# Kernel optimization log

Measured on AMD Instinct MI355X. Metric: run time of the kernel, lower is better.

The kernel has to match this reference:

```python
import jax, jax.numpy as jnp
import numpy as np

DIM = 64
HEADS = 4
EPS_LN = 1e-6
EPS_NORM = 1e-12


def _dwconv(x, w):
    # depthwise 3x3, SAME padding; x: [B,C,H,W], w: [C,1,3,3]
    return jax.lax.conv_general_dilated(
        x, w, window_strides=(1, 1), padding='SAME',
        feature_group_count=x.shape[1],
        dimension_numbers=('NCHW', 'OIHW', 'NCHW'))


def setup_inputs() -> dict:
    key = jax.random.key(0)
    ks = jax.random.split(key, 10)
    s = 0.05
    inp = {
        'x': jax.random.normal(ks[0], (8, DIM, 256, 256), dtype=jnp.float32),
        'ln_w': jnp.ones((DIM,), jnp.float32),
        'ln_b': jnp.zeros((DIM,), jnp.float32),
        'w_q': jax.random.normal(ks[1], (DIM, DIM), jnp.float32) * s,
        'w_k': jax.random.normal(ks[2], (DIM, DIM), jnp.float32) * s,
        'w_v': jax.random.normal(ks[3], (DIM, DIM), jnp.float32) * s,
        'dw_q': jax.random.normal(ks[4], (DIM, 1, 3, 3), jnp.float32) * s,
        'dw_k': jax.random.normal(ks[5], (DIM, 1, 3, 3), jnp.float32) * s,
        'dw_v': jax.random.normal(ks[6], (DIM, 1, 3, 3), jnp.float32) * s,
        'w_proj': jax.random.normal(ks[7], (DIM, DIM, 3, 3), jnp.float32) * s,
        'w_comp': jax.random.normal(ks[8], (DIM // 4, DIM), jnp.float32) * s,
        'temperature': jnp.ones((HEADS, 1, 1), jnp.float32),
    }
    return inp


def reference(x, ln_w, ln_b, w_q, w_k, w_v, dw_q, dw_k, dw_v, w_proj, w_comp, temperature):
    b, c, h, w = x.shape
    heads = temperature.shape[0]
    hd = c // heads  # per-head channels

    # LayerNorm over channel dim (per spatial location), biased variance
    mu = jnp.mean(x, axis=1, keepdims=True)
    var = jnp.mean((x - mu) ** 2, axis=1, keepdims=True)
    xn = (x - mu) / jnp.sqrt(var + EPS_LN)
    xn = xn * ln_w[None, :, None, None] + ln_b[None, :, None, None]

    # 1x1 projections then depthwise 3x3
    q = _dwconv(jnp.einsum('oc,bchw->bohw', w_q, xn), dw_q)
    k = _dwconv(jnp.einsum('oc,bchw->bohw', w_k, xn), dw_k)
    v = _dwconv(jnp.einsum('oc,bchw->bohw', w_v, xn), dw_v)

    # [b, heads, hd, h*w]
    q = q.reshape(b, heads, hd, h * w)
    k = k.reshape(b, heads, hd, h * w)
    v = v.reshape(b, heads, hd, h * w)

    # L2 normalize along spatial axis (torch F.normalize: x / max(||x||, eps))
    q = q / jnp.maximum(jnp.linalg.norm(q, axis=-1, keepdims=True), EPS_NORM)
    k = k / jnp.maximum(jnp.linalg.norm(k, axis=-1, keepdims=True), EPS_NORM)

    # channel attention: [b, heads, hd, hd]
    attn = jnp.einsum('bhcn,bhdn->bhcd', q, k) * temperature[None]
    attn = jax.nn.softmax(attn, axis=-1)
    out = jnp.einsum('bhcd,bhdn->bhcn', attn, v).reshape(b, c, h, w)

    # 3x3 projection + residual (residual is the normalized x, per source)
    out = jax.lax.conv_general_dilated(
        out, w_proj, window_strides=(1, 1), padding='SAME',
        dimension_numbers=('NCHW', 'OIHW', 'NCHW')) + xn

    # 1x1 compress to dim//4
    return jnp.einsum('oc,bchw->bohw', w_comp, out)
```

## Files before the change

kernel.cpp:

```cpp
#include <hip/hip_runtime.h>
#include <hip/hip_bf16.h>
#include <stdint.h>

#define BB 8
#define CC 64
#define HH 256
#define WW 256
#define NPIX 65536
#define HEADS 4
#define HD 16
#define PRS 76

using bf16 = __hip_bfloat16;
typedef __attribute__((ext_vector_type(8))) short short8;
typedef __attribute__((ext_vector_type(4))) float f32x4;
typedef __attribute__((ext_vector_type(2))) float f32x2;

__device__ __forceinline__ float bf2f(bf16 v) { return __bfloat162float(v); }
__device__ __forceinline__ bf16 f2bf(float v) { return __float2bfloat16(v); }
__device__ __forceinline__ short f2bfs(float f) { bf16 h = __float2bfloat16(f); return *reinterpret_cast<short*>(&h); }
__device__ __forceinline__ float bfs2f(short s) { return __uint_as_float(((uint32_t)(uint16_t)s) << 16); }
__device__ __forceinline__ uint32_t pk2(float a, float b) {
  return (uint32_t)(uint16_t)f2bfs(a) | ((uint32_t)(uint16_t)f2bfs(b) << 16);
}
__device__ __forceinline__ uint32_t pk2t(float a, float b) {
  return (__float_as_uint(a) >> 16) | (__float_as_uint(b) & 0xffff0000u);
}
__device__ __forceinline__ short8 zero8() { short8 z = {0, 0, 0, 0, 0, 0, 0, 0}; return z; }
__device__ __forceinline__ f32x2 unpk2(uint32_t w) {
  f32x2 r;
  r.x = __uint_as_float(w << 16);
  r.y = __uint_as_float(w & 0xffff0000u);
  return r;
}

__global__ void k_prep(const float* __restrict__ w_comp, const float* __restrict__ w_proj,
                       const float* __restrict__ w_q, const float* __restrict__ w_k,
                       const float* __restrict__ w_v,
                       short* __restrict__ wcpb, short* __restrict__ wqkvb,
                       short* __restrict__ wcb) {
  int idx = blockIdx.x * 256 + threadIdx.x;
  if (idx < 9 * 16 * 64) {
    int c = idx & 63;
    int o = (idx >> 6) & 15;
    int kk = idx >> 10;
    float acc = 0.f;
    for (int m = 0; m < 64; ++m)
      acc += w_comp[o * 64 + m] * w_proj[(m * 64 + c) * 9 + kk];
    wcpb[idx] = f2bfs(acc);
  }
  if (idx < 3 * 4096) {
    const float* Ws[3] = {w_q, w_k, w_v};
    wqkvb[idx] = f2bfs(Ws[idx >> 12][idx & 4095]);
  }
  if (idx < 1024) wcb[idx] = f2bfs(w_comp[idx]);
}

__global__ __launch_bounds__(256)
void k_ln(const float* __restrict__ x, const float* __restrict__ ln_w,
          const float* __restrict__ ln_b, short* __restrict__ xnb) {
  const int tid = threadIdx.x;
  const int b = blockIdx.x >> 8;
  const int n = ((blockIdx.x & 255) << 8) + tid;
  const float* xp = x + (size_t)b * CC * NPIX + n;
  float v[64];
  float s = 0.f, s2 = 0.f;
#pragma unroll
  for (int c = 0; c < 64; ++c) {
    float t0 = xp[(size_t)c * NPIX];
    v[c] = t0; s += t0; s2 += t0 * t0;
  }
  const float mu = s * (1.f / 64.f);
  const float r = rsqrtf(s2 * (1.f / 64.f) - mu * mu + 1e-6f);
  short* op = xnb + ((size_t)b * NPIX + n) * 64;
#pragma unroll
  for (int c8 = 0; c8 < 8; ++c8) {
    uint32_t pk[4];
#pragma unroll
    for (int j = 0; j < 4; ++j) {
      const int c0 = c8 * 8 + 2 * j;
      float f0 = (v[c0] - mu) * r * ln_w[c0] + ln_b[c0];
      float f1 = (v[c0 + 1] - mu) * r * ln_w[c0 + 1] + ln_b[c0 + 1];
      pk[j] = pk2(f0, f1);
    }
    *reinterpret_cast<uint4*>(op + c8 * 8) = make_uint4(pk[0], pk[1], pk[2], pk[3]);
  }
}

__global__ __launch_bounds__(512)
void k_qkv(const short* __restrict__ xnb, const short* __restrict__ wqkvb,
           const short* __restrict__ wcb,
           const float* __restrict__ dw_q, const float* __restrict__ dw_k,
           const float* __restrict__ dw_v,
           bf16* __restrict__ qo, bf16* __restrict__ ko,
           short* __restrict__ aov, short* __restrict__ res16) {
  __shared__ short pr_s[336 * PRS];
  const int tid = threadIdx.x;
  const int lane = tid & 63;
  const int wv = tid >> 6;
  const int olocal = lane & 15;
  const int g = lane >> 4;
  const int t = blockIdx.y;
  const int tx = blockIdx.x & 15, ty = (blockIdx.x >> 4) & 15, b = blockIdx.x >> 8;
  const int x0 = tx * 16 - 1, y0 = ty * 16 - 1;

  if (t == 0) {
    short8 wc0 = *reinterpret_cast<const short8*>(wcb + olocal * 64 + g * 8);
    short8 wc1 = *reinterpret_cast<const short8*>(wcb + olocal * 64 + 32 + g * 8);
#pragma unroll
    for (int t2 = 0; t2 < 2; ++t2) {
      const int oy = wv * 2 + t2;
      const int n = (ty * 16 + oy) * WW + tx * 16 + olocal;
      const short* bb = xnb + ((size_t)b * NPIX + n) * 64 + g * 8;
      short8 b0 = *reinterpret_cast<const short8*>(bb);
      short8 b1 = *reinterpret_cast<const short8*>(bb + 32);
      f32x4 acc = {0.f, 0.f, 0.f, 0.f};
      acc = __builtin_amdgcn_mfma_f32_16x16x32_bf16(wc0, b0, acc, 0, 0, 0);
      acc = __builtin_amdgcn_mfma_f32_16x16x32_bf16(wc1, b1, acc, 0, 0, 0);
      uint2 st;
      st.x = pk2(acc[0], acc[1]);
      st.y = pk2(acc[2], acc[3]);
      *reinterpret_cast<uint2*>(&res16[((size_t)b * NPIX + n) * 16 + g * 4]) = st;
    }
  }

  short8 Bt[4][2];
#pragma unroll
  for (int ot = 0; ot < 4; ++ot) {
    const short* wb = wqkvb + t * 4096 + (ot * 16 + olocal) * 64 + g * 8;
    Bt[ot][0] = *reinterpret_cast<const short8*>(wb);
    Bt[ot][1] = *reinterpret_cast<const short8*>(wb + 32);
  }

  short8 a0[3], a1[3];
#pragma unroll
  for (int j = 0; j < 3; ++j) {
    const int pt = wv + j * 8;
    const int p = pt * 16 + olocal;
    const int py = y0 + p / 18;
    const int px_ = x0 + p % 18;
    const bool vld = (pt < 21) && (p < 324) && ((unsigned)py < 256u) && ((unsigned)px_ < 256u);
    if (vld) {
      const short* ab = xnb + ((size_t)b * NPIX + py * WW + px_) * 64 + g * 8;
      a0[j] = *reinterpret_cast<const short8*>(ab);
      a1[j] = *reinterpret_cast<const short8*>(ab + 32);
    } else {
      a0[j] = zero8();
      a1[j] = zero8();
    }
  }
#pragma unroll
  for (int j = 0; j < 3; ++j) {
    const int pt = wv + j * 8;
    if (pt >= 21) continue;
    const int p2 = pt * 16 + olocal;
#pragma unroll
    for (int ot = 0; ot < 4; ++ot) {
      f32x4 acc = {0.f, 0.f, 0.f, 0.f};
      acc = __builtin_amdgcn_mfma_f32_16x16x32_bf16(Bt[ot][0], a0[j], acc, 0, 0, 0);
      acc = __builtin_amdgcn_mfma_f32_16x16x32_bf16(Bt[ot][1], a1[j], acc, 0, 0, 0);
      uint2 st;
      st.x = pk2t(acc[0], acc[1]);
      st.y = pk2t(acc[2], acc[3]);
      *reinterpret_cast<uint2*>(&pr_s[p2 * PRS + ot * 16 + g * 4]) = st;
    }
  }
  __syncthreads();

  const float* dmt = (t == 0) ? dw_q : (t == 1) ? dw_k : dw_v;
  f32x2 dm2[9][4];
#pragma unroll
  for (int u2 = 0; u2 < 4; ++u2)
#pragma unroll
    for (int kk = 0; kk < 9; ++kk) {
      dm2[kk][u2].x = dmt[(wv * 8 + 2 * u2) * 9 + kk];
      dm2[kk][u2].y = dmt[(wv * 8 + 2 * u2 + 1) * 9 + kk];
    }
  bf16* ob = ((t == 0) ? qo : ko) + (size_t)b * CC * NPIX;
#pragma unroll
  for (int i = 0; i < 4; ++i) {
    const int pxl = lane + i * 64;
    const int oy = pxl >> 4, ox = pxl & 15;
    uint4 pw[9];
#pragma unroll
    for (int ky = 0; ky < 3; ++ky)
#pragma unroll
      for (int kx = 0; kx < 3; ++kx)
        pw[ky * 3 + kx] = *reinterpret_cast<const uint4*>(
            &pr_s[((oy + ky) * 18 + ox + kx) * PRS + wv * 8]);
    f32x2 ac0 = {0.f, 0.f}, ac1 = {0.f, 0.f}, ac2 = {0.f, 0.f}, ac3 = {0.f, 0.f};
#pragma unroll
    for (int kk = 0; kk < 9; ++kk) {
      ac0 += dm2[kk][0] * unpk2(pw[kk].x);
      ac1 += dm2[kk][1] * unpk2(pw[kk].y);
      ac2 += dm2[kk][2] * unpk2(pw[kk].z);
      ac3 += dm2[kk][3] * unpk2(pw[kk].w);
    }
    const int n = (ty * 16 + oy) * WW + tx * 16 + ox;
    if (t < 2) {
      ob[(size_t)(wv * 8 + 0) * NPIX + n] = f2bf(ac0.x);
      ob[(size_t)(wv * 8 + 1) * NPIX + n] = f2bf(ac0.y);
      ob[(size_t)(wv * 8 + 2) * NPIX + n] = f2bf(ac1.x);
      ob[(size_t)(wv * 8 + 3) * NPIX + n] = f2bf(ac1.y);
      ob[(size_t)(wv * 8 + 4) * NPIX + n] = f2bf(ac2.x);
      ob[(size_t)(wv * 8 + 5) * NPIX + n] = f2bf(ac2.y);
      ob[(size_t)(wv * 8 + 6) * NPIX + n] = f2bf(ac3.x);
      ob[(size_t)(wv * 8 + 7) * NPIX + n] = f2bf(ac3.y);
    } else {
      uint4 st = make_uint4(pk2(ac0.x, ac0.y), pk2(ac1.x, ac1.y),
                            pk2(ac2.x, ac2.y), pk2(ac3.x, ac3.y));
      *reinterpret_cast<uint4*>(&aov[((size_t)b * NPIX + n) * 64 + wv * 8]) = st;
    }
  }
}

__global__ __launch_bounds__(256)
void k_logits(const bf16* __restrict__ q, const bf16* __restrict__ kk_,
              float* __restrict__ Spart, float* __restrict__ Qpart,
              float* __restrict__ Kpart) {
  const int tid = threadIdx.x;
  const int lane = tid & 63;
  const int wv = tid >> 6;
  const int bh = blockIdx.x >> 5;
  const int chunk = blockIdx.x & 31;
  const int row = lane & 15;
  const int g = lane >> 4;
  const short* qp = (const short*)q + (size_t)(bh * HD + row) * NPIX;
  const short* kp = (const short*)kk_ + (size_t)(bh * HD + row) * NPIX;
  const int n0 = chunk * 2048 + wv * 512 + g * 8;
  f32x4 s = {0.f, 0.f, 0.f, 0.f};
  f32x4 sq = {0.f, 0.f, 0.f, 0.f};
  f32x4 sk = {0.f, 0.f, 0.f, 0.f};
#pragma unroll
  for (int it = 0; it < 16; ++it) {
    const int n = n0 + it * 32;
    short8 qa = *reinterpret_cast<const short8*>(qp + n);
    short8 ka = *reinterpret_cast<const short8*>(kp + n);
    s  = __builtin_amdgcn_mfma_f32_16x16x32_bf16(qa, ka, s, 0, 0, 0);
    sq = __builtin_amdgcn_mfma_f32_16x16x32_bf16(qa, qa, sq, 0, 0, 0);
    sk = __builtin_amdgcn_mfma_f32_16x16x32_bf16(ka, ka, sk, 0, 0, 0);
  }
  const size_t tile = (size_t)blockIdx.x * 4 + wv;
  float* sp = Spart + tile * 256;
#pragma unroll
  for (int r = 0; r < 4; ++r)
    sp[(g * 4 + r) * 16 + row] = s[r];
  if ((row >> 2) == g) {
    Qpart[tile * 16 + row] = sq[row & 3];
    Kpart[tile * 16 + row] = sk[row & 3];
  }
}

__global__ __launch_bounds__(256)
void k_softmax(const float* __restrict__ Spart, const float* __restrict__ Qpart,
               const float* __restrict__ Kpart, const float* __restrict__ temp,
               short* __restrict__ attb) {
  const int tid = threadIdx.x;
  const int bh = blockIdx.x;
  const int b = bh >> 2, h = bh & 3;
  const int i = tid >> 4, j = tid & 15;
  float S = 0.f, qs = 0.f, ks = 0.f;
  const size_t t0 = (size_t)bh * 128;
  for (int c = 0; c < 128; ++c) {
    S += Spart[(t0 + c) * 256 + tid];
    qs += Qpart[(t0 + c) * 16 + i];
    ks += Kpart[(t0 + c) * 16 + j];
  }
  float nq = fmaxf(sqrtf(qs), 1e-12f);
  float nk = fmaxf(sqrtf(ks), 1e-12f);
  float val = S / (nq * nk) * temp[h];
  float m = val;
  for (int d = 1; d < 16; d <<= 1) m = fmaxf(m, __shfl_xor(m, d));
  float e = __expf(val - m);
  float s = e;
  for (int d = 1; d < 16; d <<= 1) s += __shfl_xor(s, d);
  attb[((size_t)b * 64 + h * 16 + i) * 64 + h * 16 + j] = f2bfs(e / s);
#pragma unroll
  for (int mq = 0; mq < 4; ++mq) {
    const int idx = tid * 4 + mq;
    const int r = idx >> 6, c = idx & 63;
    if ((c >> 4) != h)
      attb[((size_t)b * 64 + h * 16 + r) * 64 + c] = 0;
  }
}

__global__ __launch_bounds__(512)
void k_attf(const short* __restrict__ attb, const short* __restrict__ vao,
            const short* __restrict__ wcpb, const short* __restrict__ res16,
            float* __restrict__ out) {
  __shared__ short ao_s[336 * PRS];
  const int tid = threadIdx.x;
  const int lane = tid & 63;
  const int wv = tid >> 6;
  const int olocal = lane & 15;
  const int g = lane >> 4;
  const int tx = blockIdx.x & 15, ty = (blockIdx.x >> 4) & 15, b = blockIdx.x >> 8;
  const int x0 = tx * 16 - 1, y0 = ty * 16 - 1;

  {
    short8 AT[4][2];
#pragma unroll
    for (int ot = 0; ot < 4; ++ot) {
      const short* ab = attb + ((size_t)b * 64 + ot * 16 + olocal) * 64 + g * 8;
      AT[ot][0] = *reinterpret_cast<const short8*>(ab);
      AT[ot][1] = *reinterpret_cast<const short8*>(ab + 32);
    }
#pragma unroll
    for (int j = 0; j < 3; ++j) {
      const int pt = wv + j * 8;
      if (pt >= 21) continue;
      const int p = pt * 16 + olocal;
      const int py = y0 + p / 18;
      const int px_ = x0 + p % 18;
      const bool vld = (p < 324) && ((unsigned)py < 256u) && ((unsigned)px_ < 256u);
      short8 b0 = zero8(), b1 = zero8();
      if (vld) {
        const short* vp = vao + ((size_t)b * NPIX + py * WW + px_) * 64 + g * 8;
        b0 = *reinterpret_cast<const short8*>(vp);
        b1 = *reinterpret_cast<const short8*>(vp + 32);
      }
#pragma unroll
      for (int ot = 0; ot < 4; ++ot) {
        f32x4 acc = {0.f, 0.f, 0.f, 0.f};
        acc = __builtin_amdgcn_mfma_f32_16x16x32_bf16(AT[ot][0], b0, acc, 0, 0, 0);
        acc = __builtin_amdgcn_mfma_f32_16x16x32_bf16(AT[ot][1], b1, acc, 0, 0, 0);
        uint2 st;
        st.x = pk2t(acc[0], acc[1]);
        st.y = pk2t(acc[2], acc[3]);
        *reinterpret_cast<uint2*>(&ao_s[p * PRS + ot * 16 + g * 4]) = st;
      }
    }
  }
  __syncthreads();

  short8 WA[9][2];
#pragma unroll
  for (int kk = 0; kk < 9; ++kk) {
    const short* wb = wcpb + (kk * 16 + olocal) * 64 + g * 8;
    WA[kk][0] = *reinterpret_cast<const short8*>(wb);
    WA[kk][1] = *reinterpret_cast<const short8*>(wb + 32);
  }
#pragma unroll
  for (int s = 0; s < 2; ++s) {
    const int oy = wv * 2 + s;
    const int n0 = (ty * 16 + oy) * WW + tx * 16;
    uint2 rv = *reinterpret_cast<const uint2*>(
        &res16[((size_t)b * NPIX + n0 + olocal) * 16 + g * 4]);
    f32x4 acc;
    acc[0] = __uint_as_float(rv.x << 16);
    acc[1] = __uint_as_float(rv.x & 0xffff0000u);
    acc[2] = __uint_as_float(rv.y << 16);
    acc[3] = __uint_as_float(rv.y & 0xffff0000u);
#pragma unroll
    for (int ky = 0; ky < 3; ++ky)
#pragma unroll
      for (int kx = 0; kx < 3; ++kx) {
        const int hp = (oy + ky) * 18 + olocal + kx;
        short8 b0 = *reinterpret_cast<const short8*>(&ao_s[hp * PRS + g * 8]);
        short8 b1 = *reinterpret_cast<const short8*>(&ao_s[hp * PRS + 32 + g * 8]);
        acc = __builtin_amdgcn_mfma_f32_16x16x32_bf16(WA[ky * 3 + kx][0], b0, acc, 0, 0, 0);
        acc = __builtin_amdgcn_mfma_f32_16x16x32_bf16(WA[ky * 3 + kx][1], b1, acc, 0, 0, 0);
      }
    float* op = out + ((size_t)b * 16 + g * 4) * NPIX + n0 + olocal;
    op[0] = acc[0];
    op[NPIX] = acc[1];
    op[2 * NPIX] = acc[2];
    op[3 * NPIX] = acc[3];
  }
}

extern "C" void kernel_launch(void* const* d_in, const int* in_sizes, int n_in,
                              void* d_out, int out_size, void* d_ws, size_t ws_size,
                              hipStream_t stream) {
  const float* x      = (const float*)d_in[0];
  const float* ln_w   = (const float*)d_in[1];
  const float* ln_b   = (const float*)d_in[2];
  const float* w_q    = (const float*)d_in[3];
  const float* w_k    = (const float*)d_in[4];
  const float* w_v    = (const float*)d_in[5];
  const float* dw_q   = (const float*)d_in[6];
  const float* dw_k   = (const float*)d_in[7];
  const float* dw_v   = (const float*)d_in[8];
  const float* w_proj = (const float*)d_in[9];
  const float* w_comp = (const float*)d_in[10];
  const float* temp   = (const float*)d_in[11];
  float* out = (float*)d_out;

  const size_t SPX = (size_t)BB * NPIX;
  short* xnb   = (short*)d_ws;
  short* qb    = xnb + SPX * 64;
  short* kb    = qb + SPX * 64;
  short* aov   = kb + SPX * 64;
  short* res16 = aov + SPX * 64;
  short* wcpb  = res16 + SPX * 16;
  short* wqkvb = wcpb + 9216;
  short* wcb   = wqkvb + 12288;
  short* attb  = wcb + 1024;
  float* Spart = (float*)(attb + 8 * 64 * 64 + 512);
  float* Qpart = Spart + 4096 * 256;
  float* Kpart = Qpart + 4096 * 16;

  k_prep<<<52, 256, 0, stream>>>(w_comp, w_proj, w_q, w_k, w_v, wcpb, wqkvb, wcb);
  k_ln<<<2048, 256, 0, stream>>>(x, ln_w, ln_b, xnb);
  dim3 gqkv(2048, 3);
  k_qkv<<<gqkv, 512, 0, stream>>>(xnb, wqkvb, wcb, dw_q, dw_k, dw_v,
                                  (bf16*)qb, (bf16*)kb, aov, res16);
  k_logits<<<1024, 256, 0, stream>>>((const bf16*)qb, (const bf16*)kb, Spart, Qpart, Kpart);
  k_softmax<<<32, 256, 0, stream>>>(Spart, Qpart, Kpart, temp, attb);
  k_attf<<<2048, 512, 0, stream>>>(attb, aov, wcpb, res16, out);
}
```

Measured before the change: 310.2 us.

## Fuse Q/K Gram and norm partials into QKV kernel, drop Q/K global round trip

Q and K are now computed in the same block, one after the other, and kept on chip. Each block builds its per-tile Gram partial with MFMA in shared memory and accumulates the squared norms of Q and K. This removes the global write and re-read of the full bf16 Q and K tensors and the separate logits kernel. In exchange, shared memory grows to about 75KB, the Q/K blocks do twice the work with extra syncs, and softmax must sum 256 partials per head instead of 128.

```diff
diff --git a/kernel.cpp b/kernel.cpp
--- a/kernel.cpp
+++ b/kernel.cpp
@@ -10,6 +10,8 @@
 #define HEADS 4
 #define HD 16
 #define PRS 76
+#define QKS 268
+#define KOFF (64 * QKS)
 
 using bf16 = __hip_bfloat16;
 typedef __attribute__((ext_vector_type(8))) short short8;
@@ -87,51 +89,19 @@
   }
 }
 
-__global__ __launch_bounds__(512)
-void k_qkv(const short* __restrict__ xnb, const short* __restrict__ wqkvb,
-           const short* __restrict__ wcb,
-           const float* __restrict__ dw_q, const float* __restrict__ dw_k,
-           const float* __restrict__ dw_v,
-           bf16* __restrict__ qo, bf16* __restrict__ ko,
-           short* __restrict__ aov, short* __restrict__ res16) {
-  __shared__ short pr_s[336 * PRS];
-  const int tid = threadIdx.x;
-  const int lane = tid & 63;
-  const int wv = tid >> 6;
-  const int olocal = lane & 15;
-  const int g = lane >> 4;
-  const int t = blockIdx.y;
-  const int tx = blockIdx.x & 15, ty = (blockIdx.x >> 4) & 15, b = blockIdx.x >> 8;
-  const int x0 = tx * 16 - 1, y0 = ty * 16 - 1;
-
-  if (t == 0) {
-    short8 wc0 = *reinterpret_cast<const short8*>(wcb + olocal * 64 + g * 8);
-    short8 wc1 = *reinterpret_cast<const short8*>(wcb + olocal * 64 + 32 + g * 8);
-#pragma unroll
-    for (int t2 = 0; t2 < 2; ++t2) {
-      const int oy = wv * 2 + t2;
-      const int n = (ty * 16 + oy) * WW + tx * 16 + olocal;
-      const short* bb = xnb + ((size_t)b * NPIX + n) * 64 + g * 8;
-      short8 b0 = *reinterpret_cast<const short8*>(bb);
-      short8 b1 = *reinterpret_cast<const short8*>(bb + 32);
-      f32x4 acc = {0.f, 0.f, 0.f, 0.f};
-      acc = __builtin_amdgcn_mfma_f32_16x16x32_bf16(wc0, b0, acc, 0, 0, 0);
-      acc = __builtin_amdgcn_mfma_f32_16x16x32_bf16(wc1, b1, acc, 0, 0, 0);
-      uint2 st;
-      st.x = pk2(acc[0], acc[1]);
-      st.y = pk2(acc[2], acc[3]);
-      *reinterpret_cast<uint2*>(&res16[((size_t)b * NPIX + n) * 16 + g * 4]) = st;
-    }
-  }
-
+template <int T>
+__device__ __forceinline__ void qk_phase(
+    const short* __restrict__ xnb, const short* __restrict__ wqkvb,
+    const float* __restrict__ dmt, short* pr_s, int b, int x0, int y0,
+    int lane, int wv, int olocal, int g,
+    uint32_t (&opk)[16], float (&osq)[8]) {
   short8 Bt[4][2];
 #pragma unroll
   for (int ot = 0; ot < 4; ++ot) {
-    const short* wb = wqkvb + t * 4096 + (ot * 16 + olocal) * 64 + g * 8;
+    const short* wb = wqkvb + T * 4096 + (ot * 16 + olocal) * 64 + g * 8;
     Bt[ot][0] = *reinterpret_cast<const short8*>(wb);
     Bt[ot][1] = *reinterpret_cast<const short8*>(wb + 32);
   }
-
   short8 a0[3], a1[3];
 #pragma unroll
   for (int j = 0; j < 3; ++j) {
@@ -166,8 +136,6 @@
     }
   }
   __syncthreads();
-
-  const float* dmt = (t == 0) ? dw_q : (t == 1) ? dw_k : dw_v;
   f32x2 dm2[9][4];
 #pragma unroll
   for (int u2 = 0; u2 < 4; ++u2)
@@ -176,7 +144,6 @@
       dm2[kk][u2].x = dmt[(wv * 8 + 2 * u2) * 9 + kk];
       dm2[kk][u2].y = dmt[(wv * 8 + 2 * u2 + 1) * 9 + kk];
     }
-  bf16* ob = ((t == 0) ? qo : ko) + (size_t)b * CC * NPIX;
 #pragma unroll
   for (int i = 0; i < 4; ++i) {
     const int pxl = lane + i * 64;
@@ -196,58 +163,193 @@
       ac2 += dm2[kk][2] * unpk2(pw[kk].z);
       ac3 += dm2[kk][3] * unpk2(pw[kk].w);
     }
-    const int n = (ty * 16 + oy) * WW + tx * 16 + ox;
-    if (t < 2) {
-      ob[(size_t)(wv * 8 + 0) * NPIX + n] = f2bf(ac0.x);
-      ob[(size_t)(wv * 8 + 1) * NPIX + n] = f2bf(ac0.y);
-      ob[(size_t)(wv * 8 + 2) * NPIX + n] = f2bf(ac1.x);
-      ob[(size_t)(wv * 8 + 3) * NPIX + n] = f2bf(ac1.y);
-      ob[(size_t)(wv * 8 + 4) * NPIX + n] = f2bf(ac2.x);
-      ob[(size_t)(wv * 8 + 5) * NPIX + n] = f2bf(ac2.y);
-      ob[(size_t)(wv * 8 + 6) * NPIX + n] = f2bf(ac3.x);
-      ob[(size_t)(wv * 8 + 7) * NPIX + n] = f2bf(ac3.y);
-    } else {
+    opk[i * 4 + 0] = pk2(ac0.x, ac0.y);
+    opk[i * 4 + 1] = pk2(ac1.x, ac1.y);
+    opk[i * 4 + 2] = pk2(ac2.x, ac2.y);
+    opk[i * 4 + 3] = pk2(ac3.x, ac3.y);
+    osq[0] += ac0.x * ac0.x; osq[1] += ac0.y * ac0.y;
+    osq[2] += ac1.x * ac1.x; osq[3] += ac1.y * ac1.y;
+    osq[4] += ac2.x * ac2.x; osq[5] += ac2.y * ac2.y;
+    osq[6] += ac3.x * ac3.x; osq[7] += ac3.y * ac3.y;
+  }
+}
+
+__global__ __launch_bounds__(512)
+void k_qkgv(const short* __restrict__ xnb, const short* __restrict__ wqkvb,
+            const short* __restrict__ wcb,
+            const float* __restrict__ dw_q, const float* __restrict__ dw_k,
+            const float* __restrict__ dw_v,
+            short* __restrict__ aov, short* __restrict__ res16,
+            float* __restrict__ Spart, float* __restrict__ Qpart,
+            float* __restrict__ Kpart) {
+  __shared__ __align__(16) char smem[76800];
+  short* pr_s = (short*)smem;
+  short* qk_s = (short*)smem;
+  float* gram_s = (float*)(smem + 68608);
+  const int tid = threadIdx.x;
+  const int lane = tid & 63;
+  const int wv = tid >> 6;
+  const int olocal = lane & 15;
+  const int g = lane >> 4;
+  const int tx = blockIdx.x & 15, ty = (blockIdx.x >> 4) & 15, b = blockIdx.x >> 8;
+  const int tile = blockIdx.x & 255;
+  const int x0 = tx * 16 - 1, y0 = ty * 16 - 1;
+
+  if (blockIdx.y == 0) {
+    uint32_t qpk[16], kpk[16];
+    float sq[8] = {0.f, 0.f, 0.f, 0.f, 0.f, 0.f, 0.f, 0.f};
+    float sk[8] = {0.f, 0.f, 0.f, 0.f, 0.f, 0.f, 0.f, 0.f};
+    qk_phase<0>(xnb, wqkvb, dw_q, pr_s, b, x0, y0, lane, wv, olocal, g, qpk, sq);
+    __syncthreads();
+    qk_phase<1>(xnb, wqkvb, dw_k, pr_s, b, x0, y0, lane, wv, olocal, g, kpk, sk);
+
+#pragma unroll
+    for (int d = 1; d < 64; d <<= 1) {
+#pragma unroll
+      for (int u = 0; u < 8; ++u) {
+        sq[u] += __shfl_xor(sq[u], d);
+        sk[u] += __shfl_xor(sk[u], d);
+      }
+    }
+    if (lane == 0) {
+#pragma unroll
+      for (int u = 0; u < 8; ++u) {
+        Qpart[((size_t)b * 256 + tile) * 64 + wv * 8 + u] = sq[u];
+        Kpart[((size_t)b * 256 + tile) * 64 + wv * 8 + u] = sk[u];
+      }
+    }
+    __syncthreads();
+
+#pragma unroll
+    for (int i = 0; i < 4; ++i) {
+      const int px = lane + i * 64;
+#pragma unroll
+      for (int u2 = 0; u2 < 4; ++u2) {
+        const int ch = wv * 8 + 2 * u2;
+        const uint32_t wq = qpk[i * 4 + u2], wk = kpk[i * 4 + u2];
+        qk_s[ch * QKS + px] = (short)(wq & 0xffff);
+        qk_s[(ch + 1) * QKS + px] = (short)(wq >> 16);
+        qk_s[KOFF + ch * QKS + px] = (short)(wk & 0xffff);
+        qk_s[KOFF + (ch + 1) * QKS + px] = (short)(wk >> 16);
+      }
+    }
+    __syncthreads();
+
+    const int h = wv >> 1, half = wv & 1;
+    f32x4 sacc = {0.f, 0.f, 0.f, 0.f};
+#pragma unroll
+    for (int c4 = 0; c4 < 4; ++c4) {
+      const int chunk = half * 4 + c4;
+      const int off = (h * 16 + olocal) * QKS + chunk * 32 + g * 8;
+      short8 A = *reinterpret_cast<const short8*>(&qk_s[off]);
+      short8 Bf = *reinterpret_cast<const short8*>(&qk_s[KOFF + off]);
+      sacc = __builtin_amdgcn_mfma_f32_16x16x32_bf16(A, Bf, sacc, 0, 0, 0);
+    }
+#pragma unroll
+    for (int r = 0; r < 4; ++r)
+      gram_s[wv * 256 + (g * 4 + r) * 16 + olocal] = sacc[r];
+    __syncthreads();
+    if (!(wv & 1)) {
+#pragma unroll
+      for (int m = 0; m < 4; ++m) {
+        const int idx = lane + m * 64;
+        Spart[(((size_t)b * 256 + tile) * 4 + h) * 256 + idx] =
+            gram_s[wv * 256 + idx] + gram_s[(wv + 1) * 256 + idx];
+      }
+    }
+  } else {
+    {
+      short8 wc0 = *reinterpret_cast<const short8*>(wcb + olocal * 64 + g * 8);
+      short8 wc1 = *reinterpret_cast<const short8*>(wcb + olocal * 64 + 32 + g * 8);
+#pragma unroll
+      for (int t2 = 0; t2 < 2; ++t2) {
+        const int oy = wv * 2 + t2;
+        const int n = (ty * 16 + oy) * WW + tx * 16 + olocal;
+        const short* bb = xnb + ((size_t)b * NPIX + n) * 64 + g * 8;
+        short8 b0 = *reinterpret_cast<const short8*>(bb);
+        short8 b1 = *reinterpret_cast<const short8*>(bb + 32);
+        f32x4 acc = {0.f, 0.f, 0.f, 0.f};
+        acc = __builtin_amdgcn_mfma_f32_16x16x32_bf16(wc0, b0, acc, 0, 0, 0);
+        acc = __builtin_amdgcn_mfma_f32_16x16x32_bf16(wc1, b1, acc, 0, 0, 0);
+        uint2 st;
+        st.x = pk2(acc[0], acc[1]);
+        st.y = pk2(acc[2], acc[3]);
+        *reinterpret_cast<uint2*>(&res16[((size_t)b * NPIX + n) * 16 + g * 4]) = st;
+      }
+    }
+    short8 Bt[4][2];
+#pragma unroll
+    for (int ot = 0; ot < 4; ++ot) {
+      const short* wb = wqkvb + 2 * 4096 + (ot * 16 + olocal) * 64 + g * 8;
+      Bt[ot][0] = *reinterpret_cast<const short8*>(wb);
+      Bt[ot][1] = *reinterpret_cast<const short8*>(wb + 32);
+    }
+    short8 a0[3], a1[3];
+#pragma unroll
+    for (int j = 0; j < 3; ++j) {
+      const int pt = wv + j * 8;
+      const int p = pt * 16 + olocal;
+      const int py = y0 + p / 18;
+      const int px_ = x0 + p % 18;
+      const bool vld = (pt < 21) && (p < 324) && ((unsigned)py < 256u) && ((unsigned)px_ < 256u);
+      if (vld) {
+        const short* ab = xnb + ((size_t)b * NPIX + py * WW + px_) * 64 + g * 8;
+        a0[j] = *reinterpret_cast<const short8*>(ab);
+        a1[j] = *reinterpret_cast<const short8*>(ab + 32);
+      } else {
+        a0[j] = zero8();
+        a1[j] = zero8();
+      }
+    }
+#pragma unroll
+    for (int j = 0; j < 3; ++j) {
+      const int pt = wv + j * 8;
+      if (pt >= 21) continue;
+      const int p2 = pt * 16 + olocal;
+#pragma unroll
+      for (int ot = 0; ot < 4; ++ot) {
+        f32x4 acc = {0.f, 0.f, 0.f, 0.f};
+        acc = __builtin_amdgcn_mfma_f32_16x16x32_bf16(Bt[ot][0], a0[j], acc, 0, 0, 0);
+        acc = __builtin_amdgcn_mfma_f32_16x16x32_bf16(Bt[ot][1], a1[j], acc, 0, 0, 0);
+        uint2 st;
+        st.x = pk2t(acc[0], acc[1]);
+        st.y = pk2t(acc[2], acc[3]);
+        *reinterpret_cast<uint2*>(&pr_s[p2 * PRS + ot * 16 + g * 4]) = st;
+      }
+    }
+    __syncthreads();
+    f32x2 dm2[9][4];
+#pragma unroll
+    for (int u2 = 0; u2 < 4; ++u2)
+#pragma unroll
+      for (int kk = 0; kk < 9; ++kk) {
+        dm2[kk][u2].x = dw_v[(wv * 8 + 2 * u2) * 9 + kk];
+        dm2[kk][u2].y = dw_v[(wv * 8 + 2 * u2 + 1) * 9 + kk];
+      }
+#pragma unroll
+    for (int i = 0; i < 4; ++i) {
+      const int pxl = lane + i * 64;
+      const int oy = pxl >> 4, ox = pxl & 15;
+      uint4 pw[9];
+#pragma unroll
+      for (int ky = 0; ky < 3; ++ky)
+#pragma unroll
+        for (int kx = 0; kx < 3; ++kx)
+          pw[ky * 3 + kx] = *reinterpret_cast<const uint4*>(
+              &pr_s[((oy + ky) * 18 + ox + kx) * PRS + wv * 8]);
+      f32x2 ac0 = {0.f, 0.f}, ac1 = {0.f, 0.f}, ac2 = {0.f, 0.f}, ac3 = {0.f, 0.f};
+#pragma unroll
+      for (int kk = 0; kk < 9; ++kk) {
+        ac0 += dm2[kk][0] * unpk2(pw[kk].x);
+        ac1 += dm2[kk][1] * unpk2(pw[kk].y);
+        ac2 += dm2[kk][2] * unpk2(pw[kk].z);
+        ac3 += dm2[kk][3] * unpk2(pw[kk].w);
+      }
+      const int n = (ty * 16 + oy) * WW + tx * 16 + ox;
       uint4 st = make_uint4(pk2(ac0.x, ac0.y), pk2(ac1.x, ac1.y),
                             pk2(ac2.x, ac2.y), pk2(ac3.x, ac3.y));
       *reinterpret_cast<uint4*>(&aov[((size_t)b * NPIX + n) * 64 + wv * 8]) = st;
     }
-  }
-}
-
-__global__ __launch_bounds__(256)
-void k_logits(const bf16* __restrict__ q, const bf16* __restrict__ kk_,
-              float* __restrict__ Spart, float* __restrict__ Qpart,
-              float* __restrict__ Kpart) {
-  const int tid = threadIdx.x;
-  const int lane = tid & 63;
-  const int wv = tid >> 6;
-  const int bh = blockIdx.x >> 5;
-  const int chunk = blockIdx.x & 31;
-  const int row = lane & 15;
-  const int g = lane >> 4;
-  const short* qp = (const short*)q + (size_t)(bh * HD + row) * NPIX;
-  const short* kp = (const short*)kk_ + (size_t)(bh * HD + row) * NPIX;
-  const int n0 = chunk * 2048 + wv * 512 + g * 8;
-  f32x4 s = {0.f, 0.f, 0.f, 0.f};
-  f32x4 sq = {0.f, 0.f, 0.f, 0.f};
-  f32x4 sk = {0.f, 0.f, 0.f, 0.f};
-#pragma unroll
-  for (int it = 0; it < 16; ++it) {
-    const int n = n0 + it * 32;
-    short8 qa = *reinterpret_cast<const short8*>(qp + n);
-    short8 ka = *reinterpret_cast<const short8*>(kp + n);
-    s  = __builtin_amdgcn_mfma_f32_16x16x32_bf16(qa, ka, s, 0, 0, 0);
-    sq = __builtin_amdgcn_mfma_f32_16x16x32_bf16(qa, qa, sq, 0, 0, 0);
-    sk = __builtin_amdgcn_mfma_f32_16x16x32_bf16(ka, ka, sk, 0, 0, 0);
-  }
-  const size_t tile = (size_t)blockIdx.x * 4 + wv;
-  float* sp = Spart + tile * 256;
-#pragma unroll
-  for (int r = 0; r < 4; ++r)
-    sp[(g * 4 + r) * 16 + row] = s[r];
-  if ((row >> 2) == g) {
-    Qpart[tile * 16 + row] = sq[row & 3];
-    Kpart[tile * 16 + row] = sk[row & 3];
   }
 }
 
@@ -260,11 +362,10 @@
   const int b = bh >> 2, h = bh & 3;
   const int i = tid >> 4, j = tid & 15;
   float S = 0.f, qs = 0.f, ks = 0.f;
-  const size_t t0 = (size_t)bh * 128;
-  for (int c = 0; c < 128; ++c) {
-    S += Spart[(t0 + c) * 256 + tid];
-    qs += Qpart[(t0 + c) * 16 + i];
-    ks += Kpart[(t0 + c) * 16 + j];
+  for (int c = 0; c < 256; ++c) {
+    S += Spart[(((size_t)b * 256 + c) * 4 + h) * 256 + tid];
+    qs += Qpart[((size_t)b * 256 + c) * 64 + h * 16 + i];
+    ks += Kpart[((size_t)b * 256 + c) * 64 + h * 16 + j];
   }
   float nq = fmaxf(sqrtf(qs), 1e-12f);
   float nk = fmaxf(sqrtf(ks), 1e-12f);
@@ -388,24 +489,21 @@
 
   const size_t SPX = (size_t)BB * NPIX;
   short* xnb   = (short*)d_ws;
-  short* qb    = xnb + SPX * 64;
-  short* kb    = qb + SPX * 64;
-  short* aov   = kb + SPX * 64;
+  short* aov   = xnb + SPX * 64;
   short* res16 = aov + SPX * 64;
   short* wcpb  = res16 + SPX * 16;
   short* wqkvb = wcpb + 9216;
   short* wcb   = wqkvb + 12288;
   short* attb  = wcb + 1024;
-  float* Spart = (float*)(attb + 8 * 64 * 64 + 512);
-  float* Qpart = Spart + 4096 * 256;
-  float* Kpart = Qpart + 4096 * 16;
+  float* Spart = (float*)(attb + 32768 + 512);
+  float* Qpart = Spart + (size_t)8 * 256 * 4 * 256;
+  float* Kpart = Qpart + (size_t)8 * 256 * 64;
 
   k_prep<<<52, 256, 0, stream>>>(w_comp, w_proj, w_q, w_k, w_v, wcpb, wqkvb, wcb);
   k_ln<<<2048, 256, 0, stream>>>(x, ln_w, ln_b, xnb);
-  dim3 gqkv(2048, 3);
-  k_qkv<<<gqkv, 512, 0, stream>>>(xnb, wqkvb, wcb, dw_q, dw_k, dw_v,
-                                  (bf16*)qb, (bf16*)kb, aov, res16);
-  k_logits<<<1024, 256, 0, stream>>>((const bf16*)qb, (const bf16*)kb, Spart, Qpart, Kpart);
+  dim3 gqk(2048, 2);
+  k_qkgv<<<gqk, 512, 0, stream>>>(xnb, wqkvb, wcb, dw_q, dw_k, dw_v,
+                                  aov, res16, Spart, Qpart, Kpart);
   k_softmax<<<32, 256, 0, stream>>>(Spart, Qpart, Kpart, temp, attb);
   k_attf<<<2048, 512, 0, stream>>>(attb, aov, wcpb, res16, out);
 }
```

After: 535.4 us. 1.73x slower.
